# Kernel optimization log

Hardware: AMD Instinct MI355X
Metric: run time of the kernel (lower is better)

The kernel has to match this reference:

```python
import jax, jax.numpy as jnp
import numpy as np

B, N, D, DEG = 16, 8192, 384, 16
K, H, STEPS = 8, 128, 3


def setup_inputs() -> dict:
    key = jax.random.key(0)
    ks = jax.random.split(key, 8)
    s_in = 1.0 / np.sqrt(2 * D)
    s_h = 1.0 / np.sqrt(H)
    return {
        "q_embs": jax.random.normal(ks[0], (B, D), jnp.float32),
        "emb": jax.random.normal(ks[1], (B, N, D), jnp.float32),
        "neighbors": jax.random.randint(ks[2], (B, N, DEG), 0, N, jnp.int32),
        "labels": jax.random.randint(ks[3], (B, N), 0, 2, jnp.int32),
        "W1": jax.random.normal(ks[4], (2 * D, H), jnp.float32) * s_in,
        "b1": jnp.zeros((H,), jnp.float32),
        "W2": jax.random.normal(ks[5], (H, K), jnp.float32) * s_h,
        "b2": jnp.zeros((K,), jnp.float32),
        "P1": jax.random.normal(ks[6], (2 * D, H), jnp.float32) * s_in,
        "pb1": jnp.zeros((H,), jnp.float32),
        "P2": jax.random.normal(ks[7], (H, 1), jnp.float32) * s_h,
        "pb2": jnp.zeros((1,), jnp.float32),
    }


def reference(q_embs, emb, neighbors, labels, W1, b1, W2, b2, P1, pb1, P2, pb2):
    b, n, d = emb.shape
    k = W2.shape[1]
    # inp = [emb | q broadcast]  -> [B, N, 2D]
    inp = jnp.concatenate([emb, jnp.broadcast_to(q_embs[:, None, :], emb.shape)], axis=-1)
    # path_net: sigmoid(MLP) -> [B, N], then +1 at support (label==1) nodes
    path = jax.nn.sigmoid(jax.nn.relu(inp @ P1 + pb1) @ P2 + pb2)[..., 0]
    path = path + labels.astype(path.dtype)
    # coin_net amplitudes scaled by (1 + path)
    amps = (jax.nn.relu(inp @ W1 + b1) @ W2 + b2) * (1.0 + path)[..., None]  # [B,N,K]
    # initial uniform state
    state = jnp.full((b, n, k), 1.0 / np.sqrt(n * k), dtype=emb.dtype)

    # sparse adjacency diffusion: out[i] = sum_{j in nbrs[i]} st[j]
    spmm = jax.vmap(lambda st, nb: st[nb].sum(axis=1))  # st [N,K], nb [N,DEG]

    for _ in range(STEPS):
        st = spmm(state * amps, neighbors)                 # [B,N,K]
        norm = jnp.linalg.norm(st.reshape(b, -1), axis=1)[:, None, None]
        state = jnp.where(norm > 0, st / norm, st)
    return jnp.abs(state).sum(axis=-1)  # [B,N]
```

## Files before the change

kernel.cpp:

```cpp
#include <hip/hip_runtime.h>
#include <cstdint>
#include <cstddef>

#define BB 16
#define NN 8192
#define DD 384
#define HH 128
#define KK 8
#define DEG 16

typedef short bf8_t __attribute__((ext_vector_type(8)));
typedef float f4_t __attribute__((ext_vector_type(4)));

__device__ __forceinline__ unsigned short f2bf(float f) {
  unsigned int u = __float_as_uint(f);
  u += 0x7FFFu + ((u >> 16) & 1u);
  return (unsigned short)(u >> 16);
}

__device__ __forceinline__ bf8_t pack8(float4 f0, float4 f1) {
  union { unsigned short us[8]; bf8_t v; } pk;
  pk.us[0] = f2bf(f0.x); pk.us[1] = f2bf(f0.y);
  pk.us[2] = f2bf(f0.z); pk.us[3] = f2bf(f0.w);
  pk.us[4] = f2bf(f1.x); pk.us[5] = f2bf(f1.y);
  pk.us[6] = f2bf(f1.z); pk.us[7] = f2bf(f1.w);
  return pk.v;
}

__global__ __launch_bounds__(256) void kprep(
    const float* __restrict__ q, const float* __restrict__ W1,
    const float* __restrict__ b1, const float* __restrict__ P1,
    const float* __restrict__ pb1,
    unsigned short* __restrict__ W1t, unsigned short* __restrict__ P1t,
    float* __restrict__ base1, float* __restrict__ baseP,
    float* __restrict__ normsq)
{
  int blk = blockIdx.x, t = threadIdx.x;
  if (blk < 32) {
    int b = blk >> 1, net = blk & 1;
    const float* W = (net ? P1 : W1) + (size_t)DD * HH;
    const float* qb = q + b * DD;
    int h = t & 127, half = t >> 7;
    int d0 = half * 192;
    float a0 = 0.f, a1 = 0.f, a2 = 0.f, a3 = 0.f;
    for (int d = d0; d < d0 + 192; d += 4) {
      a0 = fmaf(qb[d],     W[(size_t)d * HH + h],       a0);
      a1 = fmaf(qb[d + 1], W[(size_t)(d + 1) * HH + h], a1);
      a2 = fmaf(qb[d + 2], W[(size_t)(d + 2) * HH + h], a2);
      a3 = fmaf(qb[d + 3], W[(size_t)(d + 3) * HH + h], a3);
    }
    __shared__ float red[256];
    red[t] = (a0 + a1) + (a2 + a3);
    __syncthreads();
    if (t < 128) {
      float tot = red[t] + red[t + 128] + (net ? pb1[h] : b1[h]);
      (net ? baseP : base1)[b * HH + h] = tot;
    }
  } else {
    int e = (blk - 32) * 3072 + t;
    for (int it = 0; it < 12; ++it, e += 256) {
      int net = e / 49152;
      int r = e - net * 49152;
      int d = r >> 7;
      int h = r & 127;
      float v = (net ? P1 : W1)[d * HH + h];
      (net ? P1t : W1t)[h * DD + d] = f2bf(v);
    }
    if (blk == 32 && t < BB) normsq[t] = 0.f;
  }
}

__global__ __launch_bounds__(256, 4) void kmlp(
    const float* __restrict__ emb, const int* __restrict__ labels,
    const unsigned short* __restrict__ W1t, const unsigned short* __restrict__ P1t,
    const float* __restrict__ base1, const float* __restrict__ baseP,
    const float* __restrict__ W2, const float* __restrict__ b2,
    const float* __restrict__ P2, const float* __restrict__ pb2,
    float* __restrict__ amps)
{
  __shared__ __align__(16) unsigned short sB[2 * 4096];
  __shared__ float sCol[128 * 4];
  __shared__ float sW2a[128 * 9];
  __shared__ float sB2[8];

  const int t = threadIdx.x;
  const int b = blockIdx.x >> 7;
  const int row0 = (blockIdx.x & 127) * 64;

  if (t < 128) {
    sCol[t * 4 + 0] = base1[b * HH + t];
    sCol[t * 4 + 1] = baseP[b * HH + t];
    sCol[t * 4 + 2] = P2[t];
  }
  for (int e = t; e < HH * KK; e += 256) {
    int h = e >> 3, kk = e & 7;
    sW2a[h * 9 + kk] = W2[e];
  }
  if (t < 8) sB2[t] = b2[t];

  const int w = t >> 6, lane = t & 63, q = lane >> 4, ln = lane & 15;
  const float* arow = emb + (size_t)(b * NN + row0 + w * 16 + ln) * DD + q * 8;

  f4_t acc1[8], accP[8];
  f4_t zero = {0.f, 0.f, 0.f, 0.f};
#pragma unroll
  for (int i = 0; i < 8; ++i) { acc1[i] = zero; accP[i] = zero; }

  float4 a0c = ((const float4*)arow)[0];
  float4 a1c = ((const float4*)arow)[1];
#pragma unroll
  for (int i = 0; i < 4; ++i) {
    int gidx = i * 256 + t;
    int net = gidx >> 9, rr = gidx & 511, h = rr >> 2, p = rr & 3;
    uint4 v = *(const uint4*)((net ? P1t : W1t) + h * DD + p * 8);
    int pos = p ^ ((h >> 1) & 3);
    *(uint4*)&sB[net * 4096 + h * 32 + pos * 8] = v;
  }

  for (int kc = 0;;) {
    __syncthreads();
    const int kn = kc + 32;
    float4 a0n, a1n;
    if (kn < DD) {
      a0n = ((const float4*)(arow + kn))[0];
      a1n = ((const float4*)(arow + kn))[1];
    }
    bf8_t af = pack8(a0c, a1c);
    const int swz = (q ^ ((ln >> 1) & 3)) * 8;
#pragma unroll
    for (int ct = 0; ct < 8; ++ct) {
      const int off = (ct * 16 + ln) * 32 + swz;
      bf8_t bf1 = *(const bf8_t*)&sB[off];
      acc1[ct] = __builtin_amdgcn_mfma_f32_16x16x32_bf16(af, bf1, acc1[ct], 0, 0, 0);
      bf8_t bfp = *(const bf8_t*)&sB[4096 + off];
      accP[ct] = __builtin_amdgcn_mfma_f32_16x16x32_bf16(af, bfp, accP[ct], 0, 0, 0);
    }
    kc = kn;
    if (kc >= DD) break;
    __syncthreads();
#pragma unroll
    for (int i = 0; i < 4; ++i) {
      int gidx = i * 256 + t;
      int net = gidx >> 9, rr = gidx & 511, h = rr >> 2, p = rr & 3;
      uint4 v = *(const uint4*)((net ? P1t : W1t) + h * DD + kc + p * 8);
      int pos = p ^ ((h >> 1) & 3);
      *(uint4*)&sB[net * 4096 + h * 32 + pos * 8] = v;
    }
    a0c = a0n; a1c = a1n;
  }

  const float pb2v = pb2[0];
#pragma unroll
  for (int r = 0; r < 4; ++r) {
    const int grow = row0 + w * 16 + q * 4 + r;
    float s[8];
#pragma unroll
    for (int kk = 0; kk < 8; ++kk) s[kk] = 0.f;
    float ps = 0.f;
#pragma unroll
    for (int ct = 0; ct < 8; ++ct) {
      int col = ct * 16 + ln;
      float h1 = fmaxf(acc1[ct][r] + sCol[col * 4 + 0], 0.f);
      float hp = fmaxf(accP[ct][r] + sCol[col * 4 + 1], 0.f);
#pragma unroll
      for (int kk = 0; kk < 8; ++kk) s[kk] = fmaf(h1, sW2a[col * 9 + kk], s[kk]);
      ps = fmaf(hp, sCol[col * 4 + 2], ps);
    }
#pragma unroll
    for (int off = 1; off < 16; off <<= 1) {
#pragma unroll
      for (int kk = 0; kk < 8; ++kk) s[kk] += __shfl_xor(s[kk], off, 64);
      ps += __shfl_xor(ps, off, 64);
    }
    if (ln == 0) {
      float path = 1.f / (1.f + __expf(-(ps + pb2v)));
      float scale = 1.f + path + (float)labels[b * NN + grow];
      float4 o0, o1;
      o0.x = (s[0] + sB2[0]) * scale; o0.y = (s[1] + sB2[1]) * scale;
      o0.z = (s[2] + sB2[2]) * scale; o0.w = (s[3] + sB2[3]) * scale;
      o1.x = (s[4] + sB2[4]) * scale; o1.y = (s[5] + sB2[5]) * scale;
      o1.z = (s[6] + sB2[6]) * scale; o1.w = (s[7] + sB2[7]) * scale;
      float4* dst = (float4*)(amps + (size_t)(b * NN + grow) * KK);
      dst[0] = o0; dst[1] = o1;
    }
  }
}

__global__ __launch_bounds__(256) void sgm(
    const int* __restrict__ nbr, const float* __restrict__ src,
    const float* __restrict__ mult, float* __restrict__ out)
{
  int idx = blockIdx.x * 256 + threadIdx.x;
  int node = idx >> 1;
  int off = (idx & 1) * 4;
  int base = node & ~(NN - 1);
  const int4* nb = (const int4*)(nbr + (size_t)node * DEG);
  float4 a = {0.f, 0.f, 0.f, 0.f};
#pragma unroll
  for (int g = 0; g < 4; ++g) {
    int4 n = nb[g];
    float4 v0 = *(const float4*)(src + (size_t)(base + n.x) * KK + off);
    float4 v1 = *(const float4*)(src + (size_t)(base + n.y) * KK + off);
    float4 v2 = *(const float4*)(src + (size_t)(base + n.z) * KK + off);
    float4 v3 = *(const float4*)(src + (size_t)(base + n.w) * KK + off);
    a.x += v0.x + v1.x + v2.x + v3.x;
    a.y += v0.y + v1.y + v2.y + v3.y;
    a.z += v0.z + v1.z + v2.z + v3.z;
    a.w += v0.w + v1.w + v2.w + v3.w;
  }
  float4 m = *(const float4*)(mult + (size_t)node * KK + off);
  a.x *= m.x; a.y *= m.y; a.z *= m.z; a.w *= m.w;
  *(float4*)(out + (size_t)node * KK + off) = a;
}

__global__ __launch_bounds__(256) void ss3(
    const int* __restrict__ nbr, const float* __restrict__ src,
    float* __restrict__ out, float* __restrict__ normsq)
{
  int idx = blockIdx.x * 256 + threadIdx.x;
  int node = idx >> 1;
  int off = (idx & 1) * 4;
  int base = node & ~(NN - 1);
  const int4* nb = (const int4*)(nbr + (size_t)node * DEG);
  float4 a = {0.f, 0.f, 0.f, 0.f};
#pragma unroll
  for (int g = 0; g < 4; ++g) {
    int4 n = nb[g];
    float4 v0 = *(const float4*)(src + (size_t)(base + n.x) * KK + off);
    float4 v1 = *(const float4*)(src + (size_t)(base + n.y) * KK + off);
    float4 v2 = *(const float4*)(src + (size_t)(base + n.z) * KK + off);
    float4 v3 = *(const float4*)(src + (size_t)(base + n.w) * KK + off);
    a.x += v0.x + v1.x + v2.x + v3.x;
    a.y += v0.y + v1.y + v2.y + v3.y;
    a.z += v0.z + v1.z + v2.z + v3.z;
    a.w += v0.w + v1.w + v2.w + v3.w;
  }
  *(float4*)(out + (size_t)node * KK + off) = a;
  float ss = a.x * a.x + a.y * a.y + a.z * a.z + a.w * a.w;
#pragma unroll
  for (int o = 1; o < 64; o <<= 1) ss += __shfl_xor(ss, o, 64);
  if ((threadIdx.x & 63) == 0) atomicAdd(&normsq[node >> 13], ss);
}

__global__ __launch_bounds__(256) void fout(
    const float* __restrict__ u, const float* __restrict__ normsq,
    float* __restrict__ out)
{
  int idx = blockIdx.x * 256 + threadIdx.x;
  float ns = normsq[idx >> 13];
  float inv = ns > 0.f ? rsqrtf(ns) : 1.f;
  const float4* p = (const float4*)(u + (size_t)idx * KK);
  float4 v0 = p[0], v1 = p[1];
  out[idx] = (fabsf(v0.x) + fabsf(v0.y) + fabsf(v0.z) + fabsf(v0.w) +
              fabsf(v1.x) + fabsf(v1.y) + fabsf(v1.z) + fabsf(v1.w)) * inv;
}

extern "C" void kernel_launch(void* const* d_in, const int* in_sizes, int n_in,
                              void* d_out, int out_size, void* d_ws, size_t ws_size,
                              hipStream_t stream) {
  const float* q   = (const float*)d_in[0];
  const float* emb = (const float*)d_in[1];
  const int*   nbr = (const int*)d_in[2];
  const int*   lab = (const int*)d_in[3];
  const float* W1  = (const float*)d_in[4];
  const float* b1  = (const float*)d_in[5];
  const float* W2  = (const float*)d_in[6];
  const float* b2  = (const float*)d_in[7];
  const float* P1  = (const float*)d_in[8];
  const float* pb1 = (const float*)d_in[9];
  const float* P2  = (const float*)d_in[10];
  const float* pb2 = (const float*)d_in[11];
  float* out = (float*)d_out;

  const size_t NK = (size_t)BB * NN * KK;
  float* ws     = (float*)d_ws;
  float* amps   = ws;
  float* uB     = amps + NK;
  float* uC     = uB + NK;
  float* base1  = uC + NK;
  float* baseP  = base1 + BB * HH;
  float* normsq = baseP + BB * HH;
  unsigned short* W1t = (unsigned short*)(normsq + 16);
  unsigned short* P1t = W1t + (size_t)HH * DD;

  kprep<<<64, 256, 0, stream>>>(q, W1, b1, P1, pb1, W1t, P1t, base1, baseP, normsq);
  kmlp<<<2048, 256, 0, stream>>>(emb, lab, W1t, P1t, base1, baseP, W2, b2, P2, pb2, amps);
  sgm<<<1024, 256, 0, stream>>>(nbr, amps, amps, uB);
  sgm<<<1024, 256, 0, stream>>>(nbr, uB, amps, uC);
  ss3<<<1024, 256, 0, stream>>>(nbr, uC, uB, normsq);
  fout<<<512, 256, 0, stream>>>(uB, normsq, out);
}
```

Measured before the change: 437.8 us.

## Split MLP nets across blocks with full-weight LDS residency and scalar gathers

Replaces the fused dual-net MLP kernel with a GEMM kernel where each block handles one net, stages the whole bf16 weight matrix in LDS, and processes 32 rows per wave with two-stage register prefetch of emb. Path scaling moves to a separate applyscale kernel. The sparse gather kernels are templated and map one feature per thread instead of four. The changes aim to remove per-chunk barriers and improve MFMA reuse, but emb may now be read twice from memory, and an extra launch plus intermediate buffer is added.

```diff
diff --git a/kernel.cpp b/kernel.cpp
--- a/kernel.cpp
+++ b/kernel.cpp
@@ -70,176 +70,183 @@
   }
 }
 
-__global__ __launch_bounds__(256, 4) void kmlp(
-    const float* __restrict__ emb, const int* __restrict__ labels,
+__global__ __launch_bounds__(512, 2) void kgemm(
+    const float* __restrict__ emb,
     const unsigned short* __restrict__ W1t, const unsigned short* __restrict__ P1t,
     const float* __restrict__ base1, const float* __restrict__ baseP,
     const float* __restrict__ W2, const float* __restrict__ b2,
     const float* __restrict__ P2, const float* __restrict__ pb2,
-    float* __restrict__ amps)
-{
-  __shared__ __align__(16) unsigned short sB[2 * 4096];
-  __shared__ float sCol[128 * 4];
+    float* __restrict__ rawamps, float* __restrict__ pslogit)
+{
+  __shared__ __align__(16) unsigned short sB[128 * 384];
   __shared__ float sW2a[128 * 9];
+  __shared__ float sBase[128];
+  __shared__ float sP2[128];
   __shared__ float sB2[8];
 
+  const int g = blockIdx.x;
+  const int slot = g & 7;
+  const int net = (g >> 3) & 1;
+  const int wid = (g >> 4) * 8 + slot;
+  const int b = wid >> 5;
+  const int rowbase = (wid & 31) * 256;
+
   const int t = threadIdx.x;
-  const int b = blockIdx.x >> 7;
-  const int row0 = (blockIdx.x & 127) * 64;
-
-  if (t < 128) {
-    sCol[t * 4 + 0] = base1[b * HH + t];
-    sCol[t * 4 + 1] = baseP[b * HH + t];
-    sCol[t * 4 + 2] = P2[t];
-  }
-  for (int e = t; e < HH * KK; e += 256) {
-    int h = e >> 3, kk = e & 7;
-    sW2a[h * 9 + kk] = W2[e];
-  }
-  if (t < 8) sB2[t] = b2[t];
-
   const int w = t >> 6, lane = t & 63, q = lane >> 4, ln = lane & 15;
-  const float* arow = emb + (size_t)(b * NN + row0 + w * 16 + ln) * DD + q * 8;
-
-  f4_t acc1[8], accP[8];
+
+  const unsigned short* Wt = net ? P1t : W1t;
+  {
+    int h = t >> 2, p0 = t & 3;
+#pragma unroll
+    for (int i = 0; i < 12; ++i) {
+      int p = p0 + i * 4;
+      uint4 v = *(const uint4*)(Wt + h * DD + p * 8);
+      *(uint4*)((char*)sB + h * 768 + ((p ^ (h & 7)) << 4)) = v;
+    }
+  }
+  if (t < 128) sBase[t] = (net ? baseP : base1)[b * HH + t];
+  if (net == 0) {
+    for (int e = t; e < HH * KK; e += 512) {
+      int h = e >> 3, kk = e & 7;
+      sW2a[h * 9 + kk] = W2[e];
+    }
+    if (t < 8) sB2[t] = b2[t];
+  } else if (t >= 128 && t < 256) {
+    sP2[t - 128] = P2[t - 128];
+  }
+
+  const float* ar0 = emb + (size_t)(b * NN + rowbase + w * 32 + ln) * DD + q * 8;
+  const float* ar1 = ar0 + (size_t)16 * DD;
+  float4 pf[2][4];
+  pf[0][0] = ((const float4*)ar0)[0];        pf[0][1] = ((const float4*)ar0)[1];
+  pf[0][2] = ((const float4*)ar1)[0];        pf[0][3] = ((const float4*)ar1)[1];
+  pf[1][0] = ((const float4*)(ar0 + 32))[0]; pf[1][1] = ((const float4*)(ar0 + 32))[1];
+  pf[1][2] = ((const float4*)(ar1 + 32))[0]; pf[1][3] = ((const float4*)(ar1 + 32))[1];
+
+  f4_t acc[2][8];
   f4_t zero = {0.f, 0.f, 0.f, 0.f};
 #pragma unroll
-  for (int i = 0; i < 8; ++i) { acc1[i] = zero; accP[i] = zero; }
-
-  float4 a0c = ((const float4*)arow)[0];
-  float4 a1c = ((const float4*)arow)[1];
-#pragma unroll
-  for (int i = 0; i < 4; ++i) {
-    int gidx = i * 256 + t;
-    int net = gidx >> 9, rr = gidx & 511, h = rr >> 2, p = rr & 3;
-    uint4 v = *(const uint4*)((net ? P1t : W1t) + h * DD + p * 8);
-    int pos = p ^ ((h >> 1) & 3);
-    *(uint4*)&sB[net * 4096 + h * 32 + pos * 8] = v;
-  }
-
-  for (int kc = 0;;) {
-    __syncthreads();
-    const int kn = kc + 32;
-    float4 a0n, a1n;
-    if (kn < DD) {
-      a0n = ((const float4*)(arow + kn))[0];
-      a1n = ((const float4*)(arow + kn))[1];
-    }
-    bf8_t af = pack8(a0c, a1c);
-    const int swz = (q ^ ((ln >> 1) & 3)) * 8;
+  for (int i = 0; i < 8; ++i) { acc[0][i] = zero; acc[1][i] = zero; }
+
+  __syncthreads();
+
+#pragma unroll
+  for (int j = 0; j < 12; ++j) {
+    const int s = j & 1;
+    bf8_t af0 = pack8(pf[s][0], pf[s][1]);
+    bf8_t af1 = pack8(pf[s][2], pf[s][3]);
+    if (j + 2 < 12) {
+      const float* p0 = ar0 + (j + 2) * 32;
+      const float* p1 = ar1 + (j + 2) * 32;
+      pf[s][0] = ((const float4*)p0)[0]; pf[s][1] = ((const float4*)p0)[1];
+      pf[s][2] = ((const float4*)p1)[0]; pf[s][3] = ((const float4*)p1)[1];
+    }
+    const int jb = j * 4;
 #pragma unroll
     for (int ct = 0; ct < 8; ++ct) {
-      const int off = (ct * 16 + ln) * 32 + swz;
-      bf8_t bf1 = *(const bf8_t*)&sB[off];
-      acc1[ct] = __builtin_amdgcn_mfma_f32_16x16x32_bf16(af, bf1, acc1[ct], 0, 0, 0);
-      bf8_t bfp = *(const bf8_t*)&sB[4096 + off];
-      accP[ct] = __builtin_amdgcn_mfma_f32_16x16x32_bf16(af, bfp, accP[ct], 0, 0, 0);
-    }
-    kc = kn;
-    if (kc >= DD) break;
-    __syncthreads();
-#pragma unroll
-    for (int i = 0; i < 4; ++i) {
-      int gidx = i * 256 + t;
-      int net = gidx >> 9, rr = gidx & 511, h = rr >> 2, p = rr & 3;
-      uint4 v = *(const uint4*)((net ? P1t : W1t) + h * DD + kc + p * 8);
-      int pos = p ^ ((h >> 1) & 3);
-      *(uint4*)&sB[net * 4096 + h * 32 + pos * 8] = v;
-    }
-    a0c = a0n; a1c = a1n;
+      const int h = ct * 16 + ln;
+      bf8_t bf = *(const bf8_t*)((const char*)sB + h * 768 + (((jb + q) ^ (ln & 7)) << 4));
+      acc[0][ct] = __builtin_amdgcn_mfma_f32_16x16x32_bf16(af0, bf, acc[0][ct], 0, 0, 0);
+      acc[1][ct] = __builtin_amdgcn_mfma_f32_16x16x32_bf16(af1, bf, acc[1][ct], 0, 0, 0);
+    }
   }
 
   const float pb2v = pb2[0];
 #pragma unroll
-  for (int r = 0; r < 4; ++r) {
-    const int grow = row0 + w * 16 + q * 4 + r;
-    float s[8];
-#pragma unroll
-    for (int kk = 0; kk < 8; ++kk) s[kk] = 0.f;
-    float ps = 0.f;
-#pragma unroll
-    for (int ct = 0; ct < 8; ++ct) {
-      int col = ct * 16 + ln;
-      float h1 = fmaxf(acc1[ct][r] + sCol[col * 4 + 0], 0.f);
-      float hp = fmaxf(accP[ct][r] + sCol[col * 4 + 1], 0.f);
-#pragma unroll
-      for (int kk = 0; kk < 8; ++kk) s[kk] = fmaf(h1, sW2a[col * 9 + kk], s[kk]);
-      ps = fmaf(hp, sCol[col * 4 + 2], ps);
-    }
-#pragma unroll
-    for (int off = 1; off < 16; off <<= 1) {
-#pragma unroll
-      for (int kk = 0; kk < 8; ++kk) s[kk] += __shfl_xor(s[kk], off, 64);
-      ps += __shfl_xor(ps, off, 64);
-    }
-    if (ln == 0) {
-      float path = 1.f / (1.f + __expf(-(ps + pb2v)));
-      float scale = 1.f + path + (float)labels[b * NN + grow];
-      float4 o0, o1;
-      o0.x = (s[0] + sB2[0]) * scale; o0.y = (s[1] + sB2[1]) * scale;
-      o0.z = (s[2] + sB2[2]) * scale; o0.w = (s[3] + sB2[3]) * scale;
-      o1.x = (s[4] + sB2[4]) * scale; o1.y = (s[5] + sB2[5]) * scale;
-      o1.z = (s[6] + sB2[6]) * scale; o1.w = (s[7] + sB2[7]) * scale;
-      float4* dst = (float4*)(amps + (size_t)(b * NN + grow) * KK);
-      dst[0] = o0; dst[1] = o1;
-    }
-  }
-}
-
-__global__ __launch_bounds__(256) void sgm(
+  for (int grp = 0; grp < 2; ++grp) {
+#pragma unroll
+    for (int r = 0; r < 4; ++r) {
+      const int grow = rowbase + w * 32 + grp * 16 + q * 4 + r;
+      if (net == 0) {
+        float s[8];
+#pragma unroll
+        for (int kk = 0; kk < 8; ++kk) s[kk] = 0.f;
+#pragma unroll
+        for (int ct = 0; ct < 8; ++ct) {
+          int col = ct * 16 + ln;
+          float h1 = fmaxf(acc[grp][ct][r] + sBase[col], 0.f);
+#pragma unroll
+          for (int kk = 0; kk < 8; ++kk) s[kk] = fmaf(h1, sW2a[col * 9 + kk], s[kk]);
+        }
+#pragma unroll
+        for (int off = 1; off < 16; off <<= 1)
+#pragma unroll
+          for (int kk = 0; kk < 8; ++kk) s[kk] += __shfl_xor(s[kk], off, 64);
+        if (ln == 0) {
+          float4 o0, o1;
+          o0.x = s[0] + sB2[0]; o0.y = s[1] + sB2[1];
+          o0.z = s[2] + sB2[2]; o0.w = s[3] + sB2[3];
+          o1.x = s[4] + sB2[4]; o1.y = s[5] + sB2[5];
+          o1.z = s[6] + sB2[6]; o1.w = s[7] + sB2[7];
+          float4* dst = (float4*)(rawamps + (size_t)(b * NN + grow) * KK);
+          dst[0] = o0; dst[1] = o1;
+        }
+      } else {
+        float ps = 0.f;
+#pragma unroll
+        for (int ct = 0; ct < 8; ++ct) {
+          int col = ct * 16 + ln;
+          float hp = fmaxf(acc[grp][ct][r] + sBase[col], 0.f);
+          ps = fmaf(hp, sP2[col], ps);
+        }
+#pragma unroll
+        for (int off = 1; off < 16; off <<= 1) ps += __shfl_xor(ps, off, 64);
+        if (ln == 0) pslogit[b * NN + grow] = ps + pb2v;
+      }
+    }
+  }
+}
+
+__global__ __launch_bounds__(256) void applyscale(
+    const float* __restrict__ raw, const float* __restrict__ psl,
+    const int* __restrict__ lab, float* __restrict__ amps)
+{
+  int node = blockIdx.x * 256 + threadIdx.x;
+  float sc = 1.f + 1.f / (1.f + __expf(-psl[node])) + (float)lab[node];
+  const float4* r = (const float4*)(raw + (size_t)node * KK);
+  float4 v0 = r[0], v1 = r[1];
+  v0.x *= sc; v0.y *= sc; v0.z *= sc; v0.w *= sc;
+  v1.x *= sc; v1.y *= sc; v1.z *= sc; v1.w *= sc;
+  float4* d = (float4*)(amps + (size_t)node * KK);
+  d[0] = v0; d[1] = v1;
+}
+
+template<bool MUL, bool NRM>
+__global__ __launch_bounds__(256) void sg8(
     const int* __restrict__ nbr, const float* __restrict__ src,
-    const float* __restrict__ mult, float* __restrict__ out)
+    const float* __restrict__ mult, float* __restrict__ out,
+    float* __restrict__ normsq)
 {
   int idx = blockIdx.x * 256 + threadIdx.x;
-  int node = idx >> 1;
-  int off = (idx & 1) * 4;
+  int node = idx >> 3, k = idx & 7;
   int base = node & ~(NN - 1);
-  const int4* nb = (const int4*)(nbr + (size_t)node * DEG);
-  float4 a = {0.f, 0.f, 0.f, 0.f};
-#pragma unroll
-  for (int g = 0; g < 4; ++g) {
-    int4 n = nb[g];
-    float4 v0 = *(const float4*)(src + (size_t)(base + n.x) * KK + off);
-    float4 v1 = *(const float4*)(src + (size_t)(base + n.y) * KK + off);
-    float4 v2 = *(const float4*)(src + (size_t)(base + n.z) * KK + off);
-    float4 v3 = *(const float4*)(src + (size_t)(base + n.w) * KK + off);
-    a.x += v0.x + v1.x + v2.x + v3.x;
-    a.y += v0.y + v1.y + v2.y + v3.y;
-    a.z += v0.z + v1.z + v2.z + v3.z;
-    a.w += v0.w + v1.w + v2.w + v3.w;
-  }
-  float4 m = *(const float4*)(mult + (size_t)node * KK + off);
-  a.x *= m.x; a.y *= m.y; a.z *= m.z; a.w *= m.w;
-  *(float4*)(out + (size_t)node * KK + off) = a;
-}
-
-__global__ __launch_bounds__(256) void ss3(
-    const int* __restrict__ nbr, const float* __restrict__ src,
-    float* __restrict__ out, float* __restrict__ normsq)
-{
-  int idx = blockIdx.x * 256 + threadIdx.x;
-  int node = idx >> 1;
-  int off = (idx & 1) * 4;
-  int base = node & ~(NN - 1);
-  const int4* nb = (const int4*)(nbr + (size_t)node * DEG);
-  float4 a = {0.f, 0.f, 0.f, 0.f};
-#pragma unroll
-  for (int g = 0; g < 4; ++g) {
-    int4 n = nb[g];
-    float4 v0 = *(const float4*)(src + (size_t)(base + n.x) * KK + off);
-    float4 v1 = *(const float4*)(src + (size_t)(base + n.y) * KK + off);
-    float4 v2 = *(const float4*)(src + (size_t)(base + n.z) * KK + off);
-    float4 v3 = *(const float4*)(src + (size_t)(base + n.w) * KK + off);
-    a.x += v0.x + v1.x + v2.x + v3.x;
-    a.y += v0.y + v1.y + v2.y + v3.y;
-    a.z += v0.z + v1.z + v2.z + v3.z;
-    a.w += v0.w + v1.w + v2.w + v3.w;
-  }
-  *(float4*)(out + (size_t)node * KK + off) = a;
-  float ss = a.x * a.x + a.y * a.y + a.z * a.z + a.w * a.w;
-#pragma unroll
-  for (int o = 1; o < 64; o <<= 1) ss += __shfl_xor(ss, o, 64);
-  if ((threadIdx.x & 63) == 0) atomicAdd(&normsq[node >> 13], ss);
+  const int4* nbp = (const int4*)(nbr + (size_t)node * DEG);
+  int4 n0 = nbp[0], n1 = nbp[1], n2 = nbp[2], n3 = nbp[3];
+  float a = 0.f;
+  a += src[(size_t)(base + n0.x) * KK + k];
+  a += src[(size_t)(base + n0.y) * KK + k];
+  a += src[(size_t)(base + n0.z) * KK + k];
+  a += src[(size_t)(base + n0.w) * KK + k];
+  a += src[(size_t)(base + n1.x) * KK + k];
+  a += src[(size_t)(base + n1.y) * KK + k];
+  a += src[(size_t)(base + n1.z) * KK + k];
+  a += src[(size_t)(base + n1.w) * KK + k];
+  a += src[(size_t)(base + n2.x) * KK + k];
+  a += src[(size_t)(base + n2.y) * KK + k];
+  a += src[(size_t)(base + n2.z) * KK + k];
+  a += src[(size_t)(base + n2.w) * KK + k];
+  a += src[(size_t)(base + n3.x) * KK + k];
+  a += src[(size_t)(base + n3.y) * KK + k];
+  a += src[(size_t)(base + n3.z) * KK + k];
+  a += src[(size_t)(base + n3.w) * KK + k];
+  if (MUL) a *= mult[(size_t)node * KK + k];
+  out[(size_t)node * KK + k] = a;
+  if (NRM) {
+    float ss = a * a;
+#pragma unroll
+    for (int o = 1; o < 64; o <<= 1) ss += __shfl_xor(ss, o, 64);
+    if ((threadIdx.x & 63) == 0) atomicAdd(&normsq[node >> 13], ss);
+  }
 }
 
 __global__ __launch_bounds__(256) void fout(
@@ -274,19 +281,22 @@
 
   const size_t NK = (size_t)BB * NN * KK;
   float* ws     = (float*)d_ws;
-  float* amps   = ws;
-  float* uB     = amps + NK;
-  float* uC     = uB + NK;
-  float* base1  = uC + NK;
+  float* buf0   = ws;
+  float* buf1   = buf0 + NK;
+  float* buf2   = buf1 + NK;
+  float* psl    = buf2 + NK;
+  float* base1  = psl + (size_t)BB * NN;
   float* baseP  = base1 + BB * HH;
   float* normsq = baseP + BB * HH;
   unsigned short* W1t = (unsigned short*)(normsq + 16);
   unsigned short* P1t = W1t + (size_t)HH * DD;
 
   kprep<<<64, 256, 0, stream>>>(q, W1, b1, P1, pb1, W1t, P1t, base1, baseP, normsq);
-  kmlp<<<2048, 256, 0, stream>>>(emb, lab, W1t, P1t, base1, baseP, W2, b2, P2, pb2, amps);
-  sgm<<<1024, 256, 0, stream>>>(nbr, amps, amps, uB);
-  sgm<<<1024, 256, 0, stream>>>(nbr, uB, amps, uC);
-  ss3<<<1024, 256, 0, stream>>>(nbr, uC, uB, normsq);
-  fout<<<512, 256, 0, stream>>>(uB, normsq, out);
-}
+  kgemm<<<1024, 512, 0, stream>>>(emb, W1t, P1t, base1, baseP, W2, b2, P2, pb2,
+                                  buf0, psl);
+  applyscale<<<512, 256, 0, stream>>>(buf0, psl, lab, buf1);
+  sg8<true, false><<<4096, 256, 0, stream>>>(nbr, buf1, buf1, buf2, normsq);
+  sg8<true, false><<<4096, 256, 0, stream>>>(nbr, buf2, buf1, buf0, normsq);
+  sg8<false, true><<<4096, 256, 0, stream>>>(nbr, buf0, buf0, buf1, normsq);
+  fout<<<512, 256, 0, stream>>>(buf1, normsq, out);
+}
```

New measurement: 612.3 us. 1.4x slower.
